# Performance work log

Measured on AMD Instinct MI355X. Metric: run time of the kernel, lower is better.

Reference implementation:

```python
import jax, jax.numpy as jnp
import numpy as np

ALPHA = 0.2
MASK_VAL = -9e15
LN_EPS = 1e-5

def leaky(x):
    return jnp.where(x >= 0, x, ALPHA * x)

def setup_inputs() -> dict:
    key = jax.random.key(0)
    ks = jax.random.split(key, 8)
    B, N, D = 4, 4096, 128
    x = jax.random.normal(ks[0], (B, N, D), dtype=jnp.float32)
    adj = jax.random.randint(ks[1], (N, N), 0, 2, dtype=jnp.int32)
    W = jax.random.normal(ks[2], (D, D), dtype=jnp.float32) * (2.0 / D) ** 0.5
    a1 = jax.random.normal(ks[3], (D, 1), dtype=jnp.float32) * (1.0 / D) ** 0.5
    a2 = jax.random.normal(ks[4], (D, 1), dtype=jnp.float32) * (1.0 / D) ** 0.5
    node_weights = jax.random.normal(ks[5], (N,), dtype=jnp.float32)
    node_bias = jnp.zeros((N,), dtype=jnp.float32)
    gamma = jnp.ones((D,), dtype=jnp.float32)
    beta = jnp.zeros((D,), dtype=jnp.float32)
    return {"x": x, "adj": adj, "W": W, "a1": a1, "a2": a2,
            "node_weights": node_weights, "node_bias": node_bias,
            "gamma": gamma, "beta": beta}

def reference(x, adj, W, a1, a2, node_weights, node_bias, gamma, beta):
    # node-wise affine + residual (dropout is identity in eval mode)
    res = x
    x = x * node_weights[None, :, None] + node_bias[None, :, None] + res  # [B,N,D]
    # linear projection + LayerNorm
    h = jnp.matmul(x, W)  # [B,N,D]
    mu = jnp.mean(h, axis=-1, keepdims=True)
    var = jnp.mean((h - mu) ** 2, axis=-1, keepdims=True)
    h = (h - mu) / jnp.sqrt(var + LN_EPS) * gamma + beta
    residential = h
    # GAT-style additive scores: e[b,i,j] = leakyrelu(f1[b,i] + f2[b,j])
    f1 = jnp.matmul(h, a1)[..., 0]  # [B,N]
    f2 = jnp.matmul(h, a2)[..., 0]  # [B,N]
    e = leaky(f1[:, :, None] + f2[:, None, :])  # [B,N,N]
    # adjacency masking (no softmax in original), second leakyrelu
    att = jnp.where(adj[None] > 0, e, MASK_VAL)
    att = leaky(att)
    h_prime = jnp.matmul(att, h)  # [B,N,D]
    return jax.nn.elu(h_prime) + residential
```

## Files before the change

### kernel.cpp

```cpp
#include <hip/hip_runtime.h>
#include <hip/hip_bf16.h>

typedef short bfrag8 __attribute__((ext_vector_type(8)));
typedef float f32x4v __attribute__((ext_vector_type(4)));
typedef unsigned short U16;
typedef unsigned int U32;

#define NN 4096
#define DD 128

static __device__ __forceinline__ U16 f2bf(float f){
  union { __hip_bfloat16 b; U16 u; } cv;
  cv.b = __float2bfloat16(f);
  return cv.u;
}

static __device__ __forceinline__ float bf2f(U32 u){
  union { float f; U32 u; } cv;
  cv.u = u << 16;
  return cv.f;
}

static __device__ __forceinline__ bfrag8 afrag(U32 word, int grp){
  U32 y = (word >> (grp*8)) & 0xffu;
  bfrag8 a;
  #pragma unroll
  for (int e = 0; e < 8; ++e) a[e] = (y & (1u<<e)) ? (short)0 : (short)0x3F80;
  return a;
}

__global__ __launch_bounds__(256) void k0_combo(const int* __restrict__ adj,
                                                U32* __restrict__ adjb,
                                                const float* __restrict__ W,
                                                U16* __restrict__ WT){
  if (blockIdx.x >= 2048){
    int i = (blockIdx.x - 2048)*256 + threadIdx.x;
    int d = i >> 7, dp = i & 127;
    WT[dp*128 + d] = f2bf(W[i]);
    return;
  }
  int gid = blockIdx.x*256 + threadIdx.x;
  const int4* src = reinterpret_cast<const int4*>(adj) + (size_t)gid*8;
  int4 v[8];
  #pragma unroll
  for (int c = 0; c < 8; ++c) v[c] = src[c];
  U32 m = 0;
  #pragma unroll
  for (int c = 0; c < 8; ++c){
    m |= (v[c].x != 0 ? 1u : 0u) << (c*4);
    m |= (v[c].y != 0 ? 2u : 0u) << (c*4);
    m |= (v[c].z != 0 ? 4u : 0u) << (c*4);
    m |= (v[c].w != 0 ? 8u : 0u) << (c*4);
  }
  adjb[gid] = m;
}

__global__ __launch_bounds__(256) void k1_prep(
    const float* __restrict__ x, const U16* __restrict__ WT,
    const float* __restrict__ nw, const float* __restrict__ nb,
    const float* __restrict__ gamma, const float* __restrict__ beta,
    U16* __restrict__ h_lnB, U16* __restrict__ hTt)
{
  __shared__ U16 lds[16384];
  const int tid = threadIdx.x;
  const int lane = tid & 63, w = tid >> 6;
  const int l15 = lane & 15, grp = lane >> 4;

  #pragma unroll
  for (int q = 0; q < 8; ++q){
    int cid = q*256 + tid;
    int dp = cid >> 4, c = cid & 15;
    *reinterpret_cast<int4*>(lds + dp*128 + ((c*8) ^ ((dp&15)<<3))) =
        *reinterpret_cast<const int4*>(WT + cid*8);
  }
  __syncthreads();

  const int rA = blockIdx.x*64 + w*16 + l15;
  const int nA = rA & 4095;
  const float wgt = nw[nA] + 1.0f, bia = nb[nA];
  const float* xr = x + (size_t)rA*DD;

  f32x4v acc[8] = {};
  #pragma unroll
  for (int ks = 0; ks < 4; ++ks){
    int d8 = ks*32 + grp*8;
    float4 xa = *reinterpret_cast<const float4*>(xr + d8);
    float4 xb = *reinterpret_cast<const float4*>(xr + d8 + 4);
    bfrag8 af;
    af[0] = (short)f2bf(xa.x*wgt + bia);
    af[1] = (short)f2bf(xa.y*wgt + bia);
    af[2] = (short)f2bf(xa.z*wgt + bia);
    af[3] = (short)f2bf(xa.w*wgt + bia);
    af[4] = (short)f2bf(xb.x*wgt + bia);
    af[5] = (short)f2bf(xb.y*wgt + bia);
    af[6] = (short)f2bf(xb.z*wgt + bia);
    af[7] = (short)f2bf(xb.w*wgt + bia);
    #pragma unroll
    for (int nf = 0; nf < 8; ++nf){
      int dp = nf*16 + l15;
      bfrag8 bf = *reinterpret_cast<const bfrag8*>(
          lds + dp*128 + ((((ks*4 + grp)*8)) ^ ((dp&15)<<3)));
      acc[nf] = __builtin_amdgcn_mfma_f32_16x16x32_bf16(af, bf, acc[nf], 0, 0, 0);
    }
  }

  float gc[8], bc[8];
  #pragma unroll
  for (int nf = 0; nf < 8; ++nf){
    int col = nf*16 + l15;
    gc[nf] = gamma[col]; bc[nf] = beta[col];
  }

  const int rCb = blockIdx.x*64 + w*16 + grp*4;
  #pragma unroll
  for (int r = 0; r < 4; ++r){
    float s = 0.f, qq = 0.f;
    #pragma unroll
    for (int nf = 0; nf < 8; ++nf){ float v = acc[nf][r]; s += v; qq += v*v; }
    #pragma unroll
    for (int m = 1; m < 16; m <<= 1){ s += __shfl_xor(s, m); qq += __shfl_xor(qq, m); }
    float mu = s * 0.0078125f;
    float var = fmaxf(qq*0.0078125f - mu*mu, 0.f);
    float rstd = rsqrtf(var + 1e-5f);
    const int rC = rCb + r;
    #pragma unroll
    for (int nf = 0; nf < 8; ++nf){
      float hn = (acc[nf][r] - mu)*rstd*gc[nf] + bc[nf];
      acc[nf][r] = hn;
      h_lnB[(size_t)rC*DD + nf*16 + l15] = f2bf(hn);
    }
  }

  __syncthreads();
  #pragma unroll
  for (int r = 0; r < 4; ++r)
    #pragma unroll
    for (int nf = 0; nf < 8; ++nf)
      lds[(w*16 + grp*4 + r)*128 + nf*16 + l15] = f2bf(acc[nf][r]);
  __syncthreads();

  {
    const int r0 = blockIdx.x*64;
    const int bB = r0 >> 12;
    const int nt0 = (r0 & 4095) >> 5;
    U16* dstt = hTt + ((size_t)(bB*128 + nt0)*128)*32;
    const int h2 = tid >> 7, d = tid & 127;
    #pragma unroll
    for (int g = 0; g < 4; ++g){
      bfrag8 v;
      #pragma unroll
      for (int e = 0; e < 8; ++e)
        v[e] = (short)lds[(h2*32 + g*8 + e)*128 + d];
      *reinterpret_cast<bfrag8*>(dstt + ((size_t)(h2*128 + d))*32 + g*8) = v;
    }
  }
}

__global__ __launch_bounds__(512, 2) void k2_main(
    const U32* __restrict__ adjb, const U16* __restrict__ hTt,
    const U16* __restrict__ h_lnB, float* __restrict__ out)
{
  __shared__ U16 part[65536];
  const int tid = threadIdx.x;
  const int lane = tid & 63, w = tid >> 6;
  const int l15 = lane & 15, grp = lane >> 4;
  const int b = blockIdx.x >> 6;
  const int iblk = (blockIdx.x & 63) * 64;
  const float CMASK = 0.2f * -9.0e15f;

  const U32* ar0 = adjb + (size_t)(iblk +      l15)*128 + w*16;
  const U32* ar1 = adjb + (size_t)(iblk + 16 + l15)*128 + w*16;
  const U32* ar2 = adjb + (size_t)(iblk + 32 + l15)*128 + w*16;
  const U32* ar3 = adjb + (size_t)(iblk + 48 + l15)*128 + w*16;

  const U16* bp = hTt + ((size_t)(b*128 + w*16)*128)*32 + l15*32 + grp*8;

  f32x4v acc[4][8] = {};

#define LOADB(P0,P1,P2,P3,P4,P5,P6,P7, S) do { \
    const U16* _q = bp + (size_t)(S)*4096; \
    P0 = *reinterpret_cast<const bfrag8*>(_q);        \
    P1 = *reinterpret_cast<const bfrag8*>(_q + 512);  \
    P2 = *reinterpret_cast<const bfrag8*>(_q + 1024); \
    P3 = *reinterpret_cast<const bfrag8*>(_q + 1536); \
    P4 = *reinterpret_cast<const bfrag8*>(_q + 2048); \
    P5 = *reinterpret_cast<const bfrag8*>(_q + 2560); \
    P6 = *reinterpret_cast<const bfrag8*>(_q + 3072); \
    P7 = *reinterpret_cast<const bfrag8*>(_q + 3584); } while(0)

#define COLM(CF, NF) do { \
    acc[0][NF] = __builtin_amdgcn_mfma_f32_16x16x32_bf16(a0, CF, acc[0][NF], 0,0,0); \
    acc[1][NF] = __builtin_amdgcn_mfma_f32_16x16x32_bf16(a1, CF, acc[1][NF], 0,0,0); \
    acc[2][NF] = __builtin_amdgcn_mfma_f32_16x16x32_bf16(a2, CF, acc[2][NF], 0,0,0); \
    acc[3][NF] = __builtin_amdgcn_mfma_f32_16x16x32_bf16(a3, CF, acc[3][NF], 0,0,0); } while(0)

#define COMPUTE(P0,P1,P2,P3,P4,P5,P6,P7, W0,W1,W2,W3) do { \
    bfrag8 a0 = afrag(W0, grp), a1 = afrag(W1, grp); \
    bfrag8 a2 = afrag(W2, grp), a3 = afrag(W3, grp); \
    COLM(P0, 0); COLM(P1, 1); COLM(P2, 2); COLM(P3, 3); \
    COLM(P4, 4); COLM(P5, 5); COLM(P6, 6); COLM(P7, 7); } while(0)

  bfrag8 A0,A1,A2,A3,A4,A5,A6,A7, B0,B1,B2,B3,B4,B5,B6,B7;
  U32 wa0,wa1,wa2,wa3, wb0,wb1,wb2,wb3;

  LOADB(A0,A1,A2,A3,A4,A5,A6,A7, 0);
  wa0 = ar0[0]; wa1 = ar1[0]; wa2 = ar2[0]; wa3 = ar3[0];

  #pragma unroll 1
  for (int it = 0; it < 8; ++it){
    const int s = it*2;
    LOADB(B0,B1,B2,B3,B4,B5,B6,B7, s+1);
    wb0 = ar0[s+1]; wb1 = ar1[s+1]; wb2 = ar2[s+1]; wb3 = ar3[s+1];
    COMPUTE(A0,A1,A2,A3,A4,A5,A6,A7, wa0,wa1,wa2,wa3);
    LOADB(A0,A1,A2,A3,A4,A5,A6,A7, s+2);
    wa0 = ar0[s+2]; wa1 = ar1[s+2]; wa2 = ar2[s+2]; wa3 = ar3[s+2];
    COMPUTE(B0,B1,B2,B3,B4,B5,B6,B7, wb0,wb1,wb2,wb3);
  }

  U16* reg = part + w*8192;
  #pragma unroll
  for (int f = 0; f < 4; ++f)
    #pragma unroll
    for (int nf = 0; nf < 8; ++nf){
      const int col = nf*16 + l15;
      #pragma unroll
      for (int r = 0; r < 4; ++r){
        const int lr = f*16 + grp*4 + r;
        reg[lr*128 + (col ^ (((lr>>2)&3)<<4))] = f2bf(acc[f][nf][r]);
      }
    }
  __syncthreads();

  #pragma unroll
  for (int rr = 0; rr < 8; ++rr){
    const int row = w*8 + rr;
    const int ci = row*64 + (lane ^ (((row>>2)&3)<<3));
    float s0 = 0.f, s1 = 0.f;
    #pragma unroll
    for (int q = 0; q < 8; ++q){
      U32 p = reinterpret_cast<const U32*>(part)[q*4096 + ci];
      s0 += bf2f(p & 0xffffu); s1 += bf2f(p >> 16);
    }
    const float h0 = CMASK * s0, h1 = CMASK * s1;
    const float e0 = h0 > 0.f ? h0 : __expf(h0) - 1.f;
    const float e1 = h1 > 0.f ? h1 : __expf(h1) - 1.f;
    const size_t o = ((size_t)b*NN + iblk + row)*DD + 2*lane;
    const U32 hl = *reinterpret_cast<const U32*>(h_lnB + o);
    float2 ov; ov.x = e0 + bf2f(hl & 0xffffu); ov.y = e1 + bf2f(hl >> 16);
    *reinterpret_cast<float2*>(out + o) = ov;
  }
}

extern "C" void kernel_launch(void* const* d_in, const int* in_sizes, int n_in,
                              void* d_out, int out_size, void* d_ws, size_t ws_size,
                              hipStream_t stream) {
  const float* x     = (const float*)d_in[0];
  const int*   adj   = (const int*)  d_in[1];
  const float* W     = (const float*)d_in[2];
  const float* nw    = (const float*)d_in[5];
  const float* nb    = (const float*)d_in[6];
  const float* gamma = (const float*)d_in[7];
  const float* beta  = (const float*)d_in[8];
  float* out = (float*)d_out;

  char* ws = (char*)d_ws;
  U16*   h_lnB = (U16*)(ws);
  U16*   hTt   = (U16*)(ws + 4*1024*1024);
  U16*   WT    = (U16*)(ws + 8*1024*1024 + 16*1024);
  U32*   adjb  = (U32*)(ws + 9*1024*1024);

  k0_combo<<<dim3(2112), dim3(256), 0, stream>>>(adj, adjb, W, WT);
  k1_prep <<<dim3(256),  dim3(256), 0, stream>>>(x, WT, nw, nb, gamma, beta,
                                                 h_lnB, hTt);
  k2_main <<<dim3(256),  dim3(512), 0, stream>>>(adjb, hTt, h_lnB, out);
}
```

Measured before the change: 52.62 us.

## Transpose packed adjacency bitmask and remap k2 blocks for XCD locality

The adjacency bitmask is stored column-group-major, so that lanes in the main kernel read consecutive words instead of row-strided ones. The k2 block index is remapped so that each XCD pair works on a single batch, which is meant to improve L2 reuse of that batch's transposed features. In exchange, the packing kernel now has each thread read a separate row, which can make the large adjacency read less coalesced.

```diff
diff --git a/kernel.cpp b/kernel.cpp
--- a/kernel.cpp
+++ b/kernel.cpp
@@ -30,7 +30,7 @@
 }
 
 __global__ __launch_bounds__(256) void k0_combo(const int* __restrict__ adj,
-                                                U32* __restrict__ adjb,
+                                                U32* __restrict__ adjbT,
                                                 const float* __restrict__ W,
                                                 U16* __restrict__ WT){
   if (blockIdx.x >= 2048){
@@ -39,8 +39,9 @@
     WT[dp*128 + d] = f2bf(W[i]);
     return;
   }
-  int gid = blockIdx.x*256 + threadIdx.x;
-  const int4* src = reinterpret_cast<const int4*>(adj) + (size_t)gid*8;
+  const int g   = blockIdx.x >> 4;
+  const int row = (blockIdx.x & 15)*256 + threadIdx.x;
+  const int4* src = reinterpret_cast<const int4*>(adj + (size_t)row*NN + g*32);
   int4 v[8];
   #pragma unroll
   for (int c = 0; c < 8; ++c) v[c] = src[c];
@@ -52,7 +53,7 @@
     m |= (v[c].z != 0 ? 4u : 0u) << (c*4);
     m |= (v[c].w != 0 ? 8u : 0u) << (c*4);
   }
-  adjb[gid] = m;
+  adjbT[(size_t)g*4096 + row] = m;
 }
 
 __global__ __launch_bounds__(256) void k1_prep(
@@ -157,21 +158,23 @@
 }
 
 __global__ __launch_bounds__(512, 2) void k2_main(
-    const U32* __restrict__ adjb, const U16* __restrict__ hTt,
+    const U32* __restrict__ adjbT, const U16* __restrict__ hTt,
     const U16* __restrict__ h_lnB, float* __restrict__ out)
 {
   __shared__ U16 part[65536];
   const int tid = threadIdx.x;
   const int lane = tid & 63, w = tid >> 6;
   const int l15 = lane & 15, grp = lane >> 4;
-  const int b = blockIdx.x >> 6;
-  const int iblk = (blockIdx.x & 63) * 64;
+  const int bid = blockIdx.x;
+  const int xcd = bid & 7;
+  const int b = xcd >> 1;
+  const int iblk = ((((bid >> 3) << 1) | (xcd & 1))) * 64;
   const float CMASK = 0.2f * -9.0e15f;
 
-  const U32* ar0 = adjb + (size_t)(iblk +      l15)*128 + w*16;
-  const U32* ar1 = adjb + (size_t)(iblk + 16 + l15)*128 + w*16;
-  const U32* ar2 = adjb + (size_t)(iblk + 32 + l15)*128 + w*16;
-  const U32* ar3 = adjb + (size_t)(iblk + 48 + l15)*128 + w*16;
+  const U32* ar0 = adjbT + (size_t)(w*16)*4096 + iblk +      l15;
+  const U32* ar1 = adjbT + (size_t)(w*16)*4096 + iblk + 16 + l15;
+  const U32* ar2 = adjbT + (size_t)(w*16)*4096 + iblk + 32 + l15;
+  const U32* ar3 = adjbT + (size_t)(w*16)*4096 + iblk + 48 + l15;
 
   const U16* bp = hTt + ((size_t)(b*128 + w*16)*128)*32 + l15*32 + grp*8;
 
@@ -210,10 +213,12 @@
   for (int it = 0; it < 8; ++it){
     const int s = it*2;
     LOADB(B0,B1,B2,B3,B4,B5,B6,B7, s+1);
-    wb0 = ar0[s+1]; wb1 = ar1[s+1]; wb2 = ar2[s+1]; wb3 = ar3[s+1];
+    wb0 = ar0[(s+1)*4096]; wb1 = ar1[(s+1)*4096];
+    wb2 = ar2[(s+1)*4096]; wb3 = ar3[(s+1)*4096];
     COMPUTE(A0,A1,A2,A3,A4,A5,A6,A7, wa0,wa1,wa2,wa3);
     LOADB(A0,A1,A2,A3,A4,A5,A6,A7, s+2);
-    wa0 = ar0[s+2]; wa1 = ar1[s+2]; wa2 = ar2[s+2]; wa3 = ar3[s+2];
+    wa0 = ar0[(s+2)*4096]; wa1 = ar1[(s+2)*4096];
+    wa2 = ar2[(s+2)*4096]; wa3 = ar3[(s+2)*4096];
     COMPUTE(B0,B1,B2,B3,B4,B5,B6,B7, wb0,wb1,wb2,wb3);
   }
 
@@ -267,10 +272,10 @@
   U16*   h_lnB = (U16*)(ws);
   U16*   hTt   = (U16*)(ws + 4*1024*1024);
   U16*   WT    = (U16*)(ws + 8*1024*1024 + 16*1024);
-  U32*   adjb  = (U32*)(ws + 9*1024*1024);
-
-  k0_combo<<<dim3(2112), dim3(256), 0, stream>>>(adj, adjb, W, WT);
+  U32*   adjbT = (U32*)(ws + 9*1024*1024);
+
+  k0_combo<<<dim3(2112), dim3(256), 0, stream>>>(adj, adjbT, W, WT);
   k1_prep <<<dim3(256),  dim3(256), 0, stream>>>(x, WT, nw, nb, gamma, beta,
                                                  h_lnB, hTt);
-  k2_main <<<dim3(256),  dim3(512), 0, stream>>>(adjb, hTt, h_lnB, out);
-}
+  k2_main <<<dim3(256),  dim3(512), 0, stream>>>(adjbT, hTt, h_lnB, out);
+}
```

Result: no change. 51.73 us (-1.7%).

## Preload adjacency bits as vector loads, unroll main loop, remap blocks per XCD

Applied to the files above, without the earlier changes.

Before the main loop, each thread reads all of its adjacency bitmask words with 128-bit int4 loads and packs the byte it needs into registers. This replaces the scalar 32-bit loads that were issued inside the loop. The main loop is now fully unrolled, so the per-step shifts become constants. Block indices are also remapped so that each XCD handles a single batch, which should keep that batch's hTt in the XCD's L2. The cost is more register pressure from the yq array and the unrolled loop, which could hurt occupancy under launch_bounds(512,2).

```diff
diff --git a/kernel.cpp b/kernel.cpp
--- a/kernel.cpp
+++ b/kernel.cpp
@@ -21,8 +21,7 @@
   return cv.f;
 }
 
-static __device__ __forceinline__ bfrag8 afrag(U32 word, int grp){
-  U32 y = (word >> (grp*8)) & 0xffu;
+static __device__ __forceinline__ bfrag8 afragb(U32 y){
   bfrag8 a;
   #pragma unroll
   for (int e = 0; e < 8; ++e) a[e] = (y & (1u<<e)) ? (short)0 : (short)0x3F80;
@@ -164,14 +163,27 @@
   const int tid = threadIdx.x;
   const int lane = tid & 63, w = tid >> 6;
   const int l15 = lane & 15, grp = lane >> 4;
-  const int b = blockIdx.x >> 6;
-  const int iblk = (blockIdx.x & 63) * 64;
+  const int bid = blockIdx.x;
+  const int xcd = bid & 7;
+  const int b = xcd >> 1;
+  const int iblk = (((bid >> 3) << 1) | (xcd & 1)) * 64;
   const float CMASK = 0.2f * -9.0e15f;
 
-  const U32* ar0 = adjb + (size_t)(iblk +      l15)*128 + w*16;
-  const U32* ar1 = adjb + (size_t)(iblk + 16 + l15)*128 + w*16;
-  const U32* ar2 = adjb + (size_t)(iblk + 32 + l15)*128 + w*16;
-  const U32* ar3 = adjb + (size_t)(iblk + 48 + l15)*128 + w*16;
+  U32 yq[4][4];
+  #pragma unroll
+  for (int f = 0; f < 4; ++f){
+    const int4* ap = reinterpret_cast<const int4*>(
+        adjb + (size_t)(iblk + f*16 + l15)*128 + w*16);
+    #pragma unroll
+    for (int q = 0; q < 4; ++q){
+      int4 v = ap[q];
+      const U32 sh = grp*8;
+      yq[f][q] = ((((U32)v.x >> sh) & 0xffu)      ) |
+                 ((((U32)v.y >> sh) & 0xffu) <<  8) |
+                 ((((U32)v.z >> sh) & 0xffu) << 16) |
+                 ((((U32)v.w >> sh) & 0xffu) << 24);
+    }
+  }
 
   const U16* bp = hTt + ((size_t)(b*128 + w*16)*128)*32 + l15*32 + grp*8;
 
@@ -194,27 +206,27 @@
     acc[2][NF] = __builtin_amdgcn_mfma_f32_16x16x32_bf16(a2, CF, acc[2][NF], 0,0,0); \
     acc[3][NF] = __builtin_amdgcn_mfma_f32_16x16x32_bf16(a3, CF, acc[3][NF], 0,0,0); } while(0)
 
-#define COMPUTE(P0,P1,P2,P3,P4,P5,P6,P7, W0,W1,W2,W3) do { \
-    bfrag8 a0 = afrag(W0, grp), a1 = afrag(W1, grp); \
-    bfrag8 a2 = afrag(W2, grp), a3 = afrag(W3, grp); \
+#define COMPUTE(P0,P1,P2,P3,P4,P5,P6,P7, Y0,Y1,Y2,Y3) do { \
+    bfrag8 a0 = afragb(Y0), a1 = afragb(Y1); \
+    bfrag8 a2 = afragb(Y2), a3 = afragb(Y3); \
     COLM(P0, 0); COLM(P1, 1); COLM(P2, 2); COLM(P3, 3); \
     COLM(P4, 4); COLM(P5, 5); COLM(P6, 6); COLM(P7, 7); } while(0)
 
   bfrag8 A0,A1,A2,A3,A4,A5,A6,A7, B0,B1,B2,B3,B4,B5,B6,B7;
-  U32 wa0,wa1,wa2,wa3, wb0,wb1,wb2,wb3;
 
   LOADB(A0,A1,A2,A3,A4,A5,A6,A7, 0);
-  wa0 = ar0[0]; wa1 = ar1[0]; wa2 = ar2[0]; wa3 = ar3[0];
-
-  #pragma unroll 1
+
+  #pragma unroll
   for (int it = 0; it < 8; ++it){
     const int s = it*2;
     LOADB(B0,B1,B2,B3,B4,B5,B6,B7, s+1);
-    wb0 = ar0[s+1]; wb1 = ar1[s+1]; wb2 = ar2[s+1]; wb3 = ar3[s+1];
-    COMPUTE(A0,A1,A2,A3,A4,A5,A6,A7, wa0,wa1,wa2,wa3);
+    COMPUTE(A0,A1,A2,A3,A4,A5,A6,A7,
+            yq[0][s>>2] >> ((s&3)*8), yq[1][s>>2] >> ((s&3)*8),
+            yq[2][s>>2] >> ((s&3)*8), yq[3][s>>2] >> ((s&3)*8));
     LOADB(A0,A1,A2,A3,A4,A5,A6,A7, s+2);
-    wa0 = ar0[s+2]; wa1 = ar1[s+2]; wa2 = ar2[s+2]; wa3 = ar3[s+2];
-    COMPUTE(B0,B1,B2,B3,B4,B5,B6,B7, wb0,wb1,wb2,wb3);
+    COMPUTE(B0,B1,B2,B3,B4,B5,B6,B7,
+            yq[0][(s+1)>>2] >> (((s+1)&3)*8), yq[1][(s+1)>>2] >> (((s+1)&3)*8),
+            yq[2][(s+1)>>2] >> (((s+1)&3)*8), yq[3][(s+1)>>2] >> (((s+1)&3)*8));
   }
 
   U16* reg = part + w*8192;
@@ -249,6 +261,9 @@
     float2 ov; ov.x = e0 + bf2f(hl & 0xffffu); ov.y = e1 + bf2f(hl >> 16);
     *reinterpret_cast<float2*>(out + o) = ov;
   }
+#undef COLM
+#undef COMPUTE
+#undef LOADB
 }
 
 extern "C" void kernel_launch(void* const* d_in, const int* in_sizes, int n_in,
```

Result: slower. 57.63 us (+9.5%).
